# Performance work log

Measured on AMD Instinct MI355X. Metric: run time of the kernel, lower is better.

## Reference

```python
import jax, jax.numpy as jnp
import numpy as np

L = 8      # num_layers (experts)
N = 8192   # tokens
H = 768    # hidden_dim
I = 1536   # inner = hidden_dim * expansion (2.0)


def setup_inputs() -> dict:
    key = jax.random.key(0)
    k = jax.random.split(key, 6)
    s1 = 1.0 / np.sqrt(H)  # torch nn.Linear default init bound (fan_in)
    s2 = 1.0 / np.sqrt(I)
    return {
        "z": jax.random.normal(k[0], (N, H), dtype=jnp.float32),
        "layer_ids": jax.random.randint(k[1], (N,), 0, L),
        "w1": jax.random.uniform(k[2], (L, H, I), jnp.float32, -s1, s1),
        "b1": jax.random.uniform(k[3], (L, I), jnp.float32, -s1, s1),
        "w2": jax.random.uniform(k[4], (L, I, H), jnp.float32, -s2, s2),
        "b2": jax.random.uniform(k[5], (L, H), jnp.float32, -s2, s2),
    }


def reference(z, layer_ids, w1, b1, w2, b2):
    # Per-token expert MLP: out[n] = z[n] + MLP_{layer_ids[n]}(z[n]).
    # Dense-all-experts formulation (jit-safe, no data-dependent shapes):
    # run every expert on all tokens, then gather each token's own expert row.
    h = jnp.einsum('nh,lhi->lni', z, w1) + b1[:, None, :]       # [L, N, I]
    a = jax.nn.gelu(h, approximate=False)                        # exact erf GELU (torch default)
    y = jnp.einsum('lni,lih->lnh', a, w2) + b2[:, None, :]       # [L, N, H]
    sel = y[layer_ids, jnp.arange(z.shape[0])]                   # [N, H] pick each token's expert
    return z + sel
```

## Files before the change

### kernel.cpp

```cpp
#include <hip/hip_runtime.h>
#include <cstdint>
#include <cstddef>

#define LNUM 8
#define NTOK 8192
#define HDIM 768
#define IDIM 1536

typedef __bf16 bf16x8 __attribute__((ext_vector_type(8)));
typedef float f32x4 __attribute__((ext_vector_type(4)));

__device__ __forceinline__ void gload16(void* lds, const void* gsrc) {
  __builtin_amdgcn_global_load_lds(
      (const __attribute__((address_space(1))) void*)gsrc,
      (__attribute__((address_space(3))) void*)lds, 16, 0, 0);
}

__device__ __forceinline__ float gelu_f(float x) {
  float xx = x * x;
  float u = x * __builtin_fmaf(0.0356774081f, xx, 0.7978845608f);
  float t = __builtin_exp2f(-2.8853900817779268f * u);
  return x * __builtin_amdgcn_rcpf(1.0f + t);
}

__device__ __forceinline__ void tr_cvt_tile(float (*tile)[65], const float* src,
                                            __bf16* dst, int R, int C, int r0,
                                            int c0, int t) {
  int rr = t >> 4, cc = (t & 15) << 2;
  #pragma unroll
  for (int it = 0; it < 4; ++it) {
    float4 v = *(const float4*)&src[(size_t)(r0 + rr + it * 16) * C + c0 + cc];
    tile[rr + it * 16][cc] = v.x;
    tile[rr + it * 16][cc + 1] = v.y;
    tile[rr + it * 16][cc + 2] = v.z;
    tile[rr + it * 16][cc + 3] = v.w;
  }
  __syncthreads();
  int c = t >> 2, rcb = (t & 3) << 3;
  #pragma unroll
  for (int it = 0; it < 2; ++it) {
    int r = rcb + it * 32;
    bf16x8 o;
    #pragma unroll
    for (int j = 0; j < 8; ++j) o[j] = (__bf16)tile[r + j][c];
    *(bf16x8*)&dst[(size_t)(c0 + c) * R + r0 + r] = o;
  }
}

#define NB_SC 32
#define NB_CZ 3072
#define NB_W 2304
__global__ __launch_bounds__(256) void prep_kernel(
    const int* __restrict__ lid, const float* __restrict__ z,
    const float* __restrict__ w1, int* __restrict__ meta,
    int* __restrict__ perm, bf16x8* __restrict__ zb, __bf16* __restrict__ w1t) {
  __shared__ float tile[64][65];
  int bxid = blockIdx.x;
  int tid = threadIdx.x;
  if (bxid < NB_SC) {
    __shared__ int ctw[4][LNUM], cbw[4][LNUM];
    __shared__ int lcnt[LNUM], lbase[LNUM];
    int b = bxid, wv = tid >> 6;
    if (tid < 32) {
      ctw[tid >> 3][tid & 7] = 0;
      cbw[tid >> 3][tid & 7] = 0;
    }
    if (tid < LNUM) lcnt[tid] = 0;
    __syncthreads();
    int cut = b << 8;
    for (int i = tid; i < NTOK; i += 256) {
      int e = lid[i];
      atomicAdd(&ctw[wv][e], 1);
      if (i < cut) atomicAdd(&cbw[wv][e], 1);
    }
    __syncthreads();
    if (tid < LNUM) {
      int e = tid, o = 0;
      for (int e2 = 0; e2 < LNUM; ++e2) {
        int s = ctw[0][e2] + ctw[1][e2] + ctw[2][e2] + ctw[3][e2];
        if (e2 < e) o += s;
      }
      lbase[e] = o + cbw[0][e] + cbw[1][e] + cbw[2][e] + cbw[3][e];
    }
    if (b == 0 && tid == 0) {
      int o = 0;
      for (int e2 = 0; e2 < LNUM; ++e2) {
        int s = ctw[0][e2] + ctw[1][e2] + ctw[2][e2] + ctw[3][e2];
        meta[e2] = o;
        o += s;
      }
      meta[8] = o;
    }
    __syncthreads();
    int i = (b << 8) + tid;
    int e = lid[i];
    int r = atomicAdd(&lcnt[e], 1);
    perm[lbase[e] + r] = i;
  } else if (bxid < NB_SC + NB_CZ) {
    int i = (bxid - NB_SC) * 256 + tid;
    const float4* zf = (const float4*)z;
    float4 a = zf[i * 2], b4 = zf[i * 2 + 1];
    bf16x8 o;
    o[0] = (__bf16)a.x; o[1] = (__bf16)a.y; o[2] = (__bf16)a.z; o[3] = (__bf16)a.w;
    o[4] = (__bf16)b4.x; o[5] = (__bf16)b4.y; o[6] = (__bf16)b4.z; o[7] = (__bf16)b4.w;
    zb[i] = o;
  } else {
    int idx = bxid - (NB_SC + NB_CZ);
    int e = idx & 7, rem = idx >> 3;
    int c0 = (rem % 24) * 64, r0 = (rem / 24) * 64;
    tr_cvt_tile(tile, w1 + (size_t)e * HDIM * IDIM, w1t + (size_t)e * HDIM * IDIM,
                HDIM, IDIM, r0, c0, tid);
  }
}

#define G1GRID 288
__global__ __launch_bounds__(512) void gemm1_kernel(
    const __bf16* __restrict__ zb, const __bf16* __restrict__ w1t,
    const float* __restrict__ b1, const int* __restrict__ meta,
    const int* __restrict__ perm, __bf16* __restrict__ act,
    const float* __restrict__ w2, __bf16* __restrict__ w2t) {
  __shared__ __align__(16) char smem[65536];
  int bid = blockIdx.x;
  int tid = threadIdx.x;
  if (bid >= G1GRID) {
    if (tid >= 256) return;
    float (*tile)[65] = (float (*)[65])smem;
    int idx = bid - G1GRID;
    int e = idx & 7, rem = idx >> 3;
    int c0 = (rem % 12) * 64, r0 = (rem / 12) * 64;
    tr_cvt_tile(tile, w2 + (size_t)e * HDIM * IDIM, w2t + (size_t)e * HDIM * IDIM,
                IDIM, HDIM, r0, c0, tid);
    return;
  }
  __bf16* As = (__bf16*)smem;
  __bf16* Bs = (__bf16*)(smem + 32768);
  const int* offs = meta;
  int e = bid & 7;
  int r = bid >> 3;
  int mt = r / 6, nt = r % 6;
  int off0 = offs[e];
  int cnt = offs[e + 1] - off0;
  if ((mt << 8) >= cnt) return;
  int row0 = off0 + (mt << 8);
  int cntRem = cnt - (mt << 8);
  if (cntRem > 256) cntRem = 256;
  int n0 = nt << 8;
  int lane = tid & 63, wv = tid >> 6;
  int wr = wv >> 2, wc = wv & 3;
  int swz = ((lane & 7) ^ (lane >> 3)) << 3;

  const __bf16* srcA[4];
  const __bf16* srcB[4];
  #pragma unroll
  for (int i = 0; i < 4; ++i) {
    int row = ((wv * 4 + i) << 3) + (lane >> 3);
    int rA = row < cntRem ? row : cntRem - 1;
    int tok = perm[row0 + rA];
    srcA[i] = zb + (size_t)tok * HDIM + swz;
    srcB[i] = w1t + ((size_t)e * IDIM + n0 + row) * HDIM + swz;
  }

  int rswz = (lane & 7) << 3;
  f32x4 acc[8][4] = {};

  for (int kk = 0; kk < HDIM / 64; ++kk) {
    #pragma unroll
    for (int i = 0; i < 4; ++i) {
      gload16(As + ((wv * 4 + i) << 9), srcA[i] + kk * 64);
      gload16(Bs + ((wv * 4 + i) << 9), srcB[i] + kk * 64);
    }
    __syncthreads();
    #pragma unroll
    for (int k2 = 0; k2 < 2; ++k2) {
      int kb = (k2 * 32 + ((lane >> 4) << 3)) ^ rswz;
      bf16x8 a[8], b[4];
      #pragma unroll
      for (int mi = 0; mi < 8; ++mi)
        a[mi] = *(const bf16x8*)&As[((wr * 128 + mi * 16 + (lane & 15)) << 6) + kb];
      #pragma unroll
      for (int ni = 0; ni < 4; ++ni)
        b[ni] = *(const bf16x8*)&Bs[((wc * 64 + ni * 16 + (lane & 15)) << 6) + kb];
      #pragma unroll
      for (int mi = 0; mi < 8; ++mi)
        #pragma unroll
        for (int ni = 0; ni < 4; ++ni)
          acc[mi][ni] = __builtin_amdgcn_mfma_f32_16x16x32_bf16(a[mi], b[ni], acc[mi][ni], 0, 0, 0);
    }
    __syncthreads();
  }

  float bb[4];
  #pragma unroll
  for (int ni = 0; ni < 4; ++ni)
    bb[ni] = b1[e * IDIM + n0 + wc * 64 + ni * 16 + (lane & 15)];

  #pragma unroll
  for (int mi = 0; mi < 8; ++mi) {
    int gr0 = wr * 128 + mi * 16 + ((lane >> 4) << 2);
    #pragma unroll
    for (int r2 = 0; r2 < 4; ++r2) {
      int g = gr0 + r2;
      if (g < cntRem) {
        size_t p = (size_t)(row0 + g);
        #pragma unroll
        for (int ni = 0; ni < 4; ++ni) {
          int col = n0 + wc * 64 + ni * 16 + (lane & 15);
          act[p * IDIM + col] = (__bf16)gelu_f(acc[mi][ni][r2] + bb[ni]);
        }
      }
    }
  }
}

#define G2GRID 288
__global__ __launch_bounds__(512) void gemm2_kernel(
    const __bf16* __restrict__ act, const __bf16* __restrict__ w2t,
    const float* __restrict__ b2, const float* __restrict__ z,
    const int* __restrict__ meta, const int* __restrict__ perm,
    float* __restrict__ out) {
  __shared__ __align__(16) char smem[49152];
  __bf16* As = (__bf16*)smem;
  __bf16* Bs = (__bf16*)(smem + 32768);
  const int* offs = meta;
  int bid = blockIdx.x;
  int e = bid & 7;
  int r = bid >> 3;
  int mt = r / 6, nt = r % 6;
  int off0 = offs[e];
  int cnt = offs[e + 1] - off0;
  if ((mt << 8) >= cnt) return;
  int row0 = off0 + (mt << 8);
  int cntRem = cnt - (mt << 8);
  if (cntRem > 256) cntRem = 256;
  int n0 = nt << 7;
  int tid = threadIdx.x, lane = tid & 63, wv = tid >> 6;
  int wr = wv >> 1, wc = wv & 1;
  int swz = ((lane & 7) ^ (lane >> 3)) << 3;

  const __bf16* srcA[4];
  const __bf16* srcB[2];
  #pragma unroll
  for (int i = 0; i < 4; ++i) {
    int row = ((wv * 4 + i) << 3) + (lane >> 3);
    int rA = row < cntRem ? row : cntRem - 1;
    srcA[i] = act + (size_t)(row0 + rA) * IDIM + swz;
  }
  #pragma unroll
  for (int i = 0; i < 2; ++i) {
    int row = ((wv * 2 + i) << 3) + (lane >> 3);
    srcB[i] = w2t + ((size_t)e * HDIM + n0 + row) * IDIM + swz;
  }

  int rswz = (lane & 7) << 3;
  f32x4 acc[4][4] = {};

  for (int kk = 0; kk < IDIM / 64; ++kk) {
    #pragma unroll
    for (int i = 0; i < 4; ++i)
      gload16(As + ((wv * 4 + i) << 9), srcA[i] + kk * 64);
    #pragma unroll
    for (int i = 0; i < 2; ++i)
      gload16(Bs + ((wv * 2 + i) << 9), srcB[i] + kk * 64);
    __syncthreads();
    #pragma unroll
    for (int k2 = 0; k2 < 2; ++k2) {
      int kb = (k2 * 32 + ((lane >> 4) << 3)) ^ rswz;
      bf16x8 a[4], b[4];
      #pragma unroll
      for (int mi = 0; mi < 4; ++mi)
        a[mi] = *(const bf16x8*)&As[((wr * 64 + mi * 16 + (lane & 15)) << 6) + kb];
      #pragma unroll
      for (int ni = 0; ni < 4; ++ni)
        b[ni] = *(const bf16x8*)&Bs[((wc * 64 + ni * 16 + (lane & 15)) << 6) + kb];
      #pragma unroll
      for (int mi = 0; mi < 4; ++mi)
        #pragma unroll
        for (int ni = 0; ni < 4; ++ni)
          acc[mi][ni] = __builtin_amdgcn_mfma_f32_16x16x32_bf16(a[mi], b[ni], acc[mi][ni], 0, 0, 0);
    }
    __syncthreads();
  }

  float bb[4];
  #pragma unroll
  for (int ni = 0; ni < 4; ++ni)
    bb[ni] = b2[e * HDIM + n0 + wc * 64 + ni * 16 + (lane & 15)];

  #pragma unroll
  for (int mi = 0; mi < 4; ++mi) {
    int gr0 = wr * 64 + mi * 16 + ((lane >> 4) << 2);
    #pragma unroll
    for (int r2 = 0; r2 < 4; ++r2) {
      int g = gr0 + r2;
      if (g < cntRem) {
        int p = row0 + g;
        int tok = perm[p];
        #pragma unroll
        for (int ni = 0; ni < 4; ++ni) {
          int col = n0 + wc * 64 + ni * 16 + (lane & 15);
          out[(size_t)tok * HDIM + col] =
              z[(size_t)tok * HDIM + col] + acc[mi][ni][r2] + bb[ni];
        }
      }
    }
  }
}

extern "C" void kernel_launch(void* const* d_in, const int* in_sizes, int n_in,
                              void* d_out, int out_size, void* d_ws, size_t ws_size,
                              hipStream_t stream) {
  const float* z  = (const float*)d_in[0];
  const int*   lid = (const int*)d_in[1];
  const float* w1 = (const float*)d_in[2];
  const float* b1 = (const float*)d_in[3];
  const float* w2 = (const float*)d_in[4];
  const float* b2 = (const float*)d_in[5];
  float* out = (float*)d_out;
  char* ws = (char*)d_ws;

  int* meta = (int*)ws;
  int* perm = (int*)(ws + 2048);
  __bf16* zb  = (__bf16*)(ws + 2048 + 32768);
  __bf16* w1t = zb + (size_t)NTOK * HDIM;
  __bf16* w2t = w1t + (size_t)LNUM * HDIM * IDIM;
  __bf16* act = w2t + (size_t)LNUM * HDIM * IDIM;

  prep_kernel<<<NB_SC + NB_CZ + NB_W, 256, 0, stream>>>(
      lid, z, w1, meta, perm, (bf16x8*)zb, w1t);
  gemm1_kernel<<<G1GRID + NB_W, 512, 0, stream>>>(zb, w1t, b1, meta, perm, act,
                                                  w2, w2t);
  gemm2_kernel<<<G2GRID, 512, 0, stream>>>(act, w2t, b2, z, meta, perm, out);
}
```

Baseline: 109.8 us.

## Double-buffer LDS tiles in both GEMMs and move w2 transpose into prep

Both GEMM kernels now keep two LDS buffers and issue the global-to-LDS loads for the next K tile before running the MFMAs on the current one. This hides global load latency behind compute and leaves one barrier per iteration. The w2 transpose-and-convert blocks move from the gemm1 launch into the prep kernel, so gemm1 runs only its GEMM tiles. The gemm2 epilogue reads the residual from the bf16 copy of z instead of the fp32 input, which cuts epilogue traffic but lowers the residual's precision. gemm1's LDS use doubles to 128KB per block, which limits occupancy to one block per CU.

```diff
diff --git a/kernel.cpp b/kernel.cpp
--- a/kernel.cpp
+++ b/kernel.cpp
@@ -52,8 +52,9 @@
 #define NB_W 2304
 __global__ __launch_bounds__(256) void prep_kernel(
     const int* __restrict__ lid, const float* __restrict__ z,
-    const float* __restrict__ w1, int* __restrict__ meta,
-    int* __restrict__ perm, bf16x8* __restrict__ zb, __bf16* __restrict__ w1t) {
+    const float* __restrict__ w1, const float* __restrict__ w2,
+    int* __restrict__ meta, int* __restrict__ perm, bf16x8* __restrict__ zb,
+    __bf16* __restrict__ w1t, __bf16* __restrict__ w2t) {
   __shared__ float tile[64][65];
   int bxid = blockIdx.x;
   int tid = threadIdx.x;
@@ -104,12 +105,18 @@
     o[0] = (__bf16)a.x; o[1] = (__bf16)a.y; o[2] = (__bf16)a.z; o[3] = (__bf16)a.w;
     o[4] = (__bf16)b4.x; o[5] = (__bf16)b4.y; o[6] = (__bf16)b4.z; o[7] = (__bf16)b4.w;
     zb[i] = o;
-  } else {
+  } else if (bxid < NB_SC + NB_CZ + NB_W) {
     int idx = bxid - (NB_SC + NB_CZ);
     int e = idx & 7, rem = idx >> 3;
     int c0 = (rem % 24) * 64, r0 = (rem / 24) * 64;
     tr_cvt_tile(tile, w1 + (size_t)e * HDIM * IDIM, w1t + (size_t)e * HDIM * IDIM,
                 HDIM, IDIM, r0, c0, tid);
+  } else {
+    int idx = bxid - (NB_SC + NB_CZ + NB_W);
+    int e = idx & 7, rem = idx >> 3;
+    int c0 = (rem % 12) * 64, r0 = (rem / 12) * 64;
+    tr_cvt_tile(tile, w2 + (size_t)e * HDIM * IDIM, w2t + (size_t)e * HDIM * IDIM,
+                IDIM, HDIM, r0, c0, tid);
   }
 }
 
@@ -117,24 +124,11 @@
 __global__ __launch_bounds__(512) void gemm1_kernel(
     const __bf16* __restrict__ zb, const __bf16* __restrict__ w1t,
     const float* __restrict__ b1, const int* __restrict__ meta,
-    const int* __restrict__ perm, __bf16* __restrict__ act,
-    const float* __restrict__ w2, __bf16* __restrict__ w2t) {
-  __shared__ __align__(16) char smem[65536];
+    const int* __restrict__ perm, __bf16* __restrict__ act) {
+  __shared__ __bf16 As[2][256 * 64];
+  __shared__ __bf16 Bs[2][256 * 64];
+  const int* offs = meta;
   int bid = blockIdx.x;
-  int tid = threadIdx.x;
-  if (bid >= G1GRID) {
-    if (tid >= 256) return;
-    float (*tile)[65] = (float (*)[65])smem;
-    int idx = bid - G1GRID;
-    int e = idx & 7, rem = idx >> 3;
-    int c0 = (rem % 12) * 64, r0 = (rem / 12) * 64;
-    tr_cvt_tile(tile, w2 + (size_t)e * HDIM * IDIM, w2t + (size_t)e * HDIM * IDIM,
-                IDIM, HDIM, r0, c0, tid);
-    return;
-  }
-  __bf16* As = (__bf16*)smem;
-  __bf16* Bs = (__bf16*)(smem + 32768);
-  const int* offs = meta;
   int e = bid & 7;
   int r = bid >> 3;
   int mt = r / 6, nt = r % 6;
@@ -145,7 +139,7 @@
   int cntRem = cnt - (mt << 8);
   if (cntRem > 256) cntRem = 256;
   int n0 = nt << 8;
-  int lane = tid & 63, wv = tid >> 6;
+  int tid = threadIdx.x, lane = tid & 63, wv = tid >> 6;
   int wr = wv >> 2, wc = wv & 3;
   int swz = ((lane & 7) ^ (lane >> 3)) << 3;
 
@@ -163,23 +157,33 @@
   int rswz = (lane & 7) << 3;
   f32x4 acc[8][4] = {};
 
-  for (int kk = 0; kk < HDIM / 64; ++kk) {
-    #pragma unroll
-    for (int i = 0; i < 4; ++i) {
-      gload16(As + ((wv * 4 + i) << 9), srcA[i] + kk * 64);
-      gload16(Bs + ((wv * 4 + i) << 9), srcB[i] + kk * 64);
-    }
-    __syncthreads();
+  const int NT = HDIM / 64;
+  #pragma unroll
+  for (int i = 0; i < 4; ++i) {
+    gload16((char*)As[0] + ((wv * 4 + i) << 10), srcA[i]);
+    gload16((char*)Bs[0] + ((wv * 4 + i) << 10), srcB[i]);
+  }
+  __syncthreads();
+
+  int cur = 0;
+  for (int kk = 0; kk < NT; ++kk) {
+    if (kk + 1 < NT) {
+      #pragma unroll
+      for (int i = 0; i < 4; ++i) {
+        gload16((char*)As[cur ^ 1] + ((wv * 4 + i) << 10), srcA[i] + (kk + 1) * 64);
+        gload16((char*)Bs[cur ^ 1] + ((wv * 4 + i) << 10), srcB[i] + (kk + 1) * 64);
+      }
+    }
     #pragma unroll
     for (int k2 = 0; k2 < 2; ++k2) {
       int kb = (k2 * 32 + ((lane >> 4) << 3)) ^ rswz;
       bf16x8 a[8], b[4];
       #pragma unroll
       for (int mi = 0; mi < 8; ++mi)
-        a[mi] = *(const bf16x8*)&As[((wr * 128 + mi * 16 + (lane & 15)) << 6) + kb];
+        a[mi] = *(const bf16x8*)&As[cur][((wr * 128 + mi * 16 + (lane & 15)) << 6) + kb];
       #pragma unroll
       for (int ni = 0; ni < 4; ++ni)
-        b[ni] = *(const bf16x8*)&Bs[((wc * 64 + ni * 16 + (lane & 15)) << 6) + kb];
+        b[ni] = *(const bf16x8*)&Bs[cur][((wc * 64 + ni * 16 + (lane & 15)) << 6) + kb];
       #pragma unroll
       for (int mi = 0; mi < 8; ++mi)
         #pragma unroll
@@ -187,6 +191,7 @@
           acc[mi][ni] = __builtin_amdgcn_mfma_f32_16x16x32_bf16(a[mi], b[ni], acc[mi][ni], 0, 0, 0);
     }
     __syncthreads();
+    cur ^= 1;
   }
 
   float bb[4];
@@ -215,12 +220,11 @@
 #define G2GRID 288
 __global__ __launch_bounds__(512) void gemm2_kernel(
     const __bf16* __restrict__ act, const __bf16* __restrict__ w2t,
-    const float* __restrict__ b2, const float* __restrict__ z,
+    const float* __restrict__ b2, const __bf16* __restrict__ zb,
     const int* __restrict__ meta, const int* __restrict__ perm,
     float* __restrict__ out) {
-  __shared__ __align__(16) char smem[49152];
-  __bf16* As = (__bf16*)smem;
-  __bf16* Bs = (__bf16*)(smem + 32768);
+  __shared__ __bf16 As[2][256 * 64];
+  __shared__ __bf16 Bs[2][128 * 64];
   const int* offs = meta;
   int bid = blockIdx.x;
   int e = bid & 7;
@@ -254,24 +258,35 @@
   int rswz = (lane & 7) << 3;
   f32x4 acc[4][4] = {};
 
-  for (int kk = 0; kk < IDIM / 64; ++kk) {
-    #pragma unroll
-    for (int i = 0; i < 4; ++i)
-      gload16(As + ((wv * 4 + i) << 9), srcA[i] + kk * 64);
-    #pragma unroll
-    for (int i = 0; i < 2; ++i)
-      gload16(Bs + ((wv * 2 + i) << 9), srcB[i] + kk * 64);
-    __syncthreads();
+  const int NT = IDIM / 64;
+  #pragma unroll
+  for (int i = 0; i < 4; ++i)
+    gload16((char*)As[0] + ((wv * 4 + i) << 10), srcA[i]);
+  #pragma unroll
+  for (int i = 0; i < 2; ++i)
+    gload16((char*)Bs[0] + ((wv * 2 + i) << 10), srcB[i]);
+  __syncthreads();
+
+  int cur = 0;
+  for (int kk = 0; kk < NT; ++kk) {
+    if (kk + 1 < NT) {
+      #pragma unroll
+      for (int i = 0; i < 4; ++i)
+        gload16((char*)As[cur ^ 1] + ((wv * 4 + i) << 10), srcA[i] + (kk + 1) * 64);
+      #pragma unroll
+      for (int i = 0; i < 2; ++i)
+        gload16((char*)Bs[cur ^ 1] + ((wv * 2 + i) << 10), srcB[i] + (kk + 1) * 64);
+    }
     #pragma unroll
     for (int k2 = 0; k2 < 2; ++k2) {
       int kb = (k2 * 32 + ((lane >> 4) << 3)) ^ rswz;
       bf16x8 a[4], b[4];
       #pragma unroll
       for (int mi = 0; mi < 4; ++mi)
-        a[mi] = *(const bf16x8*)&As[((wr * 64 + mi * 16 + (lane & 15)) << 6) + kb];
+        a[mi] = *(const bf16x8*)&As[cur][((wr * 64 + mi * 16 + (lane & 15)) << 6) + kb];
       #pragma unroll
       for (int ni = 0; ni < 4; ++ni)
-        b[ni] = *(const bf16x8*)&Bs[((wc * 64 + ni * 16 + (lane & 15)) << 6) + kb];
+        b[ni] = *(const bf16x8*)&Bs[cur][((wc * 64 + ni * 16 + (lane & 15)) << 6) + kb];
       #pragma unroll
       for (int mi = 0; mi < 4; ++mi)
         #pragma unroll
@@ -279,6 +294,7 @@
           acc[mi][ni] = __builtin_amdgcn_mfma_f32_16x16x32_bf16(a[mi], b[ni], acc[mi][ni], 0, 0, 0);
     }
     __syncthreads();
+    cur ^= 1;
   }
 
   float bb[4];
@@ -299,7 +315,7 @@
         for (int ni = 0; ni < 4; ++ni) {
           int col = n0 + wc * 64 + ni * 16 + (lane & 15);
           out[(size_t)tok * HDIM + col] =
-              z[(size_t)tok * HDIM + col] + acc[mi][ni][r2] + bb[ni];
+              (float)zb[(size_t)tok * HDIM + col] + acc[mi][ni][r2] + bb[ni];
         }
       }
     }
@@ -325,9 +341,8 @@
   __bf16* w2t = w1t + (size_t)LNUM * HDIM * IDIM;
   __bf16* act = w2t + (size_t)LNUM * HDIM * IDIM;
 
-  prep_kernel<<<NB_SC + NB_CZ + NB_W, 256, 0, stream>>>(
-      lid, z, w1, meta, perm, (bf16x8*)zb, w1t);
-  gemm1_kernel<<<G1GRID + NB_W, 512, 0, stream>>>(zb, w1t, b1, meta, perm, act,
-                                                  w2, w2t);
-  gemm2_kernel<<<G2GRID, 512, 0, stream>>>(act, w2t, b2, z, meta, perm, out);
-}
+  prep_kernel<<<NB_SC + NB_CZ + 2 * NB_W, 256, 0, stream>>>(
+      lid, z, w1, w2, meta, perm, (bf16x8*)zb, w1t, w2t);
+  gemm1_kernel<<<G1GRID, 512, 0, stream>>>(zb, w1t, b1, meta, perm, act);
+  gemm2_kernel<<<G2GRID, 512, 0, stream>>>(act, w2t, b2, zb, meta, perm, out);
+}
```

Result: faster. 106.5 us (-3.0%).
